# Kernel optimization log

Hardware: AMD Instinct MI355X
Metric: run time of the kernel (lower is better)

The kernel has to match this reference:

```python
import jax, jax.numpy as jnp
import numpy as np

EPS = 1e-8
WINDOW = 3      # config.router_window_size
TEMP = 1.0      # config.router_temp (> 0, so sqrt(D) fallback unused)
TOP_K = 2       # config.moe_top_k


def _routing_weights(x, prototypes):
    # L2-normalize router input per token (normalize_router_input=True)
    x = x / jnp.clip(jnp.linalg.norm(x, axis=-1, keepdims=True), EPS)
    # 'window' mode: causal moving average of size WINDOW along seq, with the
    # first token replicated WINDOW-1 times on the left (matches F.conv1d with
    # left pad of flat_input[:, :, [0]] and an averaging kernel).
    w = WINDOW
    padded = jnp.concatenate([jnp.repeat(x[:, :1], w - 1, axis=1), x], axis=1)  # [B, S+w-1, D]
    cs = jnp.concatenate(
        [jnp.zeros_like(padded[:, :1]), jnp.cumsum(padded, axis=1)], axis=1
    )  # [B, S+w, D]
    router_input = (cs[:, w:] - cs[:, :-w]) / w  # [B, S, D] moving mean
    # F.linear(router_input, prototypes): logits over experts
    logits = jnp.einsum('bsd,ed->bse', router_input, prototypes)  # [B, S, E]
    # softmax in float32 (F.softmax(..., dtype=torch.float))
    return jax.nn.softmax((logits / TEMP).astype(jnp.float32), axis=-1)


def setup_inputs() -> dict:
    key = jax.random.key(0)
    k1, k2 = jax.random.split(key)
    bs, sq, D, E = 8, 2048, 1024, 64
    x = jax.random.normal(k1, (bs, sq, D), dtype=jnp.float32)
    prototypes = jax.random.normal(k2, (E, D), dtype=jnp.float32) * 0.02
    attn_mask = jnp.ones((bs, sq), dtype=jnp.int32)
    return {"x": x, "prototypes": prototypes, "attn_mask": attn_mask}


def reference(x, prototypes, attn_mask):
    # attn_mask is all ones here; in 'window' mode it only feeds logging stats.
    routing_weights = _routing_weights(x, prototypes)          # [B, S, E]
    weights, modules = jax.lax.top_k(routing_weights, TOP_K)   # [B, S, K]
    weights = weights / weights.sum(axis=-1, keepdims=True)    # renormalize top-k
    return modules, weights
```

## Files before the change

### kernel.cpp

```cpp
#include <hip/hip_runtime.h>
#include <math.h>


#define BB 8
#define SS 2048
#define DD 1024
#define EE 64
#define EPSV 1e-8f

#define FMA4(A, s, P) \
  A.x += (s) * (P).x; A.y += (s) * (P).y; A.z += (s) * (P).z; A.w += (s) * (P).w;

#define SUMSQ4(v) ((v).x * (v).x + (v).y * (v).y + (v).z * (v).z + (v).w * (v).w)

__global__ __launch_bounds__(256) void repack_proto(
    const float* __restrict__ proto, float* __restrict__ ptt) {
  const int gid = blockIdx.x * 256 + threadIdx.x;
  const int d = gid >> 6;
  const int e = gid & 63;
  ptt[gid] = proto[(size_t)e * DD + d];
}

__global__ __launch_bounds__(512) void router_dots(
    const float* __restrict__ x, const float* __restrict__ ptt,
    float* __restrict__ dots) {
  __shared__ float SMEM[9216];

  const int tid  = threadIdx.x;
  const int lane = tid & 63;
  const int w    = __builtin_amdgcn_readfirstlane(tid >> 6);
  const int eg   = lane & 7;
  const int tg   = lane >> 3;
  const int b    = blockIdx.x >> 5;
  const int s0   = (blockIdx.x & 31) * 64;

  float* xtw = SMEM + w * 544;
  float* ptw = SMEM + 4352 + w * 512;
  float* nqp = SMEM + 8704;

  const int kbase = w * 128;
  const float* xsrow = x + ((size_t)b * SS + s0 + lane) * DD + kbase;
  const float* psrow = ptt + (size_t)kbase * EE + lane * 4;

  float4 accA0[4], accA1[4], accB0[4], accB1[4];
#pragma unroll
  for (int i = 0; i < 4; ++i) {
    accA0[i] = make_float4(0.f, 0.f, 0.f, 0.f);
    accA1[i] = make_float4(0.f, 0.f, 0.f, 0.f);
    accB0[i] = make_float4(0.f, 0.f, 0.f, 0.f);
    accB1[i] = make_float4(0.f, 0.f, 0.f, 0.f);
  }
  float q = 0.0f;

  {
    const float4 v0 = *(const float4*)(xsrow);
    const float4 v1 = *(const float4*)(xsrow + 4);
    const float4 r0 = *(const float4*)(psrow);
    const float4 r1 = *(const float4*)(psrow + 256);
    q += SUMSQ4(v0) + SUMSQ4(v1);
    float* d = xtw + lane;
    d[0]   = v0.x; d[68]  = v0.y; d[136] = v0.z; d[204] = v0.w;
    d[272] = v1.x; d[340] = v1.y; d[408] = v1.z; d[476] = v1.w;
    *(float4*)(ptw + lane * 4)       = r0;
    *(float4*)(ptw + 256 + lane * 4) = r1;
  }

  const float* xc = xtw + tg * 8;
  const float* pc = ptw + eg * 8;

  for (int c = 0; c < 16; ++c) {
    float4 v0, v1, r0, r1;
    if (c + 1 < 16) {
      v0 = *(const float4*)(xsrow + (c + 1) * 8);
      v1 = *(const float4*)(xsrow + (c + 1) * 8 + 4);
      r0 = *(const float4*)(psrow + (c + 1) * 512);
      r1 = *(const float4*)(psrow + (c + 1) * 512 + 256);
    }
#pragma unroll
    for (int kk = 0; kk < 8; ++kk) {
      const float4 xfA = *(const float4*)(xc + kk * 68);
      const float4 xfB = *(const float4*)(xc + kk * 68 + 4);
      const float4 p0  = *(const float4*)(pc + kk * 64);
      const float4 p1  = *(const float4*)(pc + kk * 64 + 4);
      FMA4(accA0[0], xfA.x, p0) FMA4(accA1[0], xfA.x, p1)
      FMA4(accA0[1], xfA.y, p0) FMA4(accA1[1], xfA.y, p1)
      FMA4(accA0[2], xfA.z, p0) FMA4(accA1[2], xfA.z, p1)
      FMA4(accA0[3], xfA.w, p0) FMA4(accA1[3], xfA.w, p1)
      FMA4(accB0[0], xfB.x, p0) FMA4(accB1[0], xfB.x, p1)
      FMA4(accB0[1], xfB.y, p0) FMA4(accB1[1], xfB.y, p1)
      FMA4(accB0[2], xfB.z, p0) FMA4(accB1[2], xfB.z, p1)
      FMA4(accB0[3], xfB.w, p0) FMA4(accB1[3], xfB.w, p1)
    }
    if (c + 1 < 16) {
      q += SUMSQ4(v0) + SUMSQ4(v1);
      float* d = xtw + lane;
      d[0]   = v0.x; d[68]  = v0.y; d[136] = v0.z; d[204] = v0.w;
      d[272] = v1.x; d[340] = v1.y; d[408] = v1.z; d[476] = v1.w;
      *(float4*)(ptw + lane * 4)       = r0;
      *(float4*)(ptw + 256 + lane * 4) = r1;
    }
  }

  nqp[w * 64 + lane] = q;

  float* B0 = SMEM;
  float* B1 = SMEM + 4352;

#define WRB(R)                                                        \
  { _Pragma("unroll") for (int i = 0; i < 4; ++i) {                   \
      float* pA_ = (R) + (tg * 8 + i) * 68 + eg * 8;                  \
      float* pB_ = (R) + (tg * 8 + 4 + i) * 68 + eg * 8;              \
      *(float4*)(pA_)     = accA0[i];                                 \
      *(float4*)(pA_ + 4) = accA1[i];                                 \
      *(float4*)(pB_)     = accB0[i];                                 \
      *(float4*)(pB_ + 4) = accB1[i]; } }
#define ADDB(R)                                                       \
  { _Pragma("unroll") for (int i = 0; i < 4; ++i) {                   \
      const float* pA_ = (R) + (tg * 8 + i) * 68 + eg * 8;            \
      const float* pB_ = (R) + (tg * 8 + 4 + i) * 68 + eg * 8;        \
      const float4 tA0 = *(const float4*)(pA_);                       \
      const float4 tA1 = *(const float4*)(pA_ + 4);                   \
      const float4 tB0 = *(const float4*)(pB_);                       \
      const float4 tB1 = *(const float4*)(pB_ + 4);                   \
      accA0[i].x += tA0.x; accA0[i].y += tA0.y;                       \
      accA0[i].z += tA0.z; accA0[i].w += tA0.w;                       \
      accA1[i].x += tA1.x; accA1[i].y += tA1.y;                       \
      accA1[i].z += tA1.z; accA1[i].w += tA1.w;                       \
      accB0[i].x += tB0.x; accB0[i].y += tB0.y;                       \
      accB0[i].z += tB0.z; accB0[i].w += tB0.w;                       \
      accB1[i].x += tB1.x; accB1[i].y += tB1.y;                       \
      accB1[i].z += tB1.z; accB1[i].w += tB1.w; } }

  __syncthreads();
  if (w == 1) WRB(B0)
  if (w == 5) WRB(B1)
  __syncthreads();
  if (w == 0) ADDB(B0)
  if (w == 4) ADDB(B1)
  __syncthreads();
  if (w == 3) WRB(B0)
  if (w == 7) WRB(B1)
  __syncthreads();
  if (w == 2) ADDB(B0)
  if (w == 6) ADDB(B1)
  __syncthreads();
  if (w == 2) WRB(B0)
  if (w == 6) WRB(B1)
  __syncthreads();
  if (w == 0) ADDB(B0)
  if (w == 4) ADDB(B1)
  __syncthreads();
  if (w == 4) WRB(B0)
  __syncthreads();
  if (w == 0) {
    ADDB(B0)
#pragma unroll
    for (int i = 0; i < 4; ++i) {
      const int rA = tg * 8 + i;
      const int rB = rA + 4;
      float qsA = 0.0f, qsB = 0.0f;
#pragma unroll
      for (int ww = 0; ww < 8; ++ww) {
        qsA += nqp[ww * 64 + rA];
        qsB += nqp[ww * 64 + rB];
      }
      const float invA = 1.0f / fmaxf(sqrtf(qsA), EPSV);
      const float invB = 1.0f / fmaxf(sqrtf(qsB), EPSV);
      float4 oA0 = accA0[i], oA1 = accA1[i], oB0 = accB0[i], oB1 = accB1[i];
      oA0.x *= invA; oA0.y *= invA; oA0.z *= invA; oA0.w *= invA;
      oA1.x *= invA; oA1.y *= invA; oA1.z *= invA; oA1.w *= invA;
      oB0.x *= invB; oB0.y *= invB; oB0.z *= invB; oB0.w *= invB;
      oB1.x *= invB; oB1.y *= invB; oB1.z *= invB; oB1.w *= invB;
      float* dpA = dots + ((size_t)b * SS + s0 + rA) * EE + eg * 8;
      float* dpB = dots + ((size_t)b * SS + s0 + rB) * EE + eg * 8;
      *(float4*)(dpA)     = oA0;
      *(float4*)(dpA + 4) = oA1;
      *(float4*)(dpB)     = oB0;
      *(float4*)(dpB + 4) = oB1;
    }
  }
}

#define T2UP(s, ei)                                            \
  if ((s) > v1) { v2 = v1; i2 = i1; v1 = (s); i1 = (ei); }     \
  else if ((s) > v2) { v2 = (s); i2 = (ei); }

__global__ __launch_bounds__(256) void router_top2(
    const float* __restrict__ dots, float* __restrict__ out) {
  const int gtid = blockIdx.x * 256 + threadIdx.x;
  const int tok  = gtid >> 3;
  const int h    = gtid & 7;
  const int b    = tok >> 11;
  const int sl   = tok & (SS - 1);
  const int r0   = (sl >= 2) ? sl - 2 : 0;
  const int r1   = (sl >= 1) ? sl - 1 : 0;

  const float* d0 = dots + ((size_t)b * SS + r0) * EE + h * 8;
  const float* d1 = dots + ((size_t)b * SS + r1) * EE + h * 8;
  const float* d2 = dots + ((size_t)b * SS + sl) * EE + h * 8;

  float v1 = -INFINITY, v2 = -INFINITY;
  int i1 = 0, i2 = 0;
#pragma unroll
  for (int qd = 0; qd < 2; ++qd) {
    const float4 a = *(const float4*)(d0 + qd * 4);
    const float4 c = *(const float4*)(d1 + qd * 4);
    const float4 e = *(const float4*)(d2 + qd * 4);
    const int e0 = h * 8 + qd * 4;
    float s;
    s = a.x + c.x + e.x; T2UP(s, e0 + 0)
    s = a.y + c.y + e.y; T2UP(s, e0 + 1)
    s = a.z + c.z + e.z; T2UP(s, e0 + 2)
    s = a.w + c.w + e.w; T2UP(s, e0 + 3)
  }

#pragma unroll
  for (int m = 1; m <= 4; m <<= 1) {
    const float ov1 = __shfl_xor(v1, m);
    const int   oi1 = __shfl_xor(i1, m);
    const float ov2 = __shfl_xor(v2, m);
    const int   oi2 = __shfl_xor(i2, m);
    const bool o_beats = (ov1 > v1) || (ov1 == v1 && oi1 < i1);
    if (o_beats) {
      const bool v1_beats_o2 = (v1 > ov2) || (v1 == ov2 && i1 < oi2);
      v2 = v1_beats_o2 ? v1 : ov2;
      i2 = v1_beats_o2 ? i1 : oi2;
      v1 = ov1;
      i1 = oi1;
    } else {
      const bool o1_beats_v2 = (ov1 > v2) || (ov1 == v2 && oi1 < i2);
      if (o1_beats_v2) { v2 = ov1; i2 = oi1; }
    }
  }

  if (h == 0) {
    const float ex = expf((v2 - v1) * (1.0f / 3.0f));
    const float w1 = 1.0f / (1.0f + ex);
    const size_t o = (size_t)tok * 2;
    *(float2*)(out + o) = make_float2((float)i1, (float)i2);
    *(float2*)(out + (size_t)BB * SS * 2 + o) = make_float2(w1, ex * w1);
  }
}

extern "C" void kernel_launch(void* const* d_in, const int* in_sizes, int n_in,
                              void* d_out, int out_size, void* d_ws, size_t ws_size,
                              hipStream_t stream) {
  const float* x     = (const float*)d_in[0];
  const float* proto = (const float*)d_in[1];
  float* out  = (float*)d_out;
  float* ptt  = (float*)d_ws;
  float* dots = (float*)((char*)d_ws + (512 << 10));

  repack_proto<<<dim3(256), dim3(256), 0, stream>>>(proto, ptt);
  router_dots<<<dim3(256), dim3(512), 0, stream>>>(x, ptt, dots);
  router_top2<<<dim3(512), dim3(256), 0, stream>>>(dots, out);
}
```

Baseline: 126.8 us.

## Split router dot K-dimension across sixteen waves per block instead of eight

The router_dots kernel now launches 1024 threads per block, and each of 16 waves handles a 64-wide slice of D instead of a 128-wide slice, halving the per-wave inner loop. Shared memory grows to hold the extra per-wave tiles, and the cross-wave reduction tree is extended to 16 partial sums. The aim is more memory-level parallelism per CU, since the grid has only 256 blocks. The cost is more reduction stages with extra barriers, plus tighter register limits under the larger launch bound.

```diff
diff --git a/kernel.cpp b/kernel.cpp
--- a/kernel.cpp
+++ b/kernel.cpp
@@ -21,10 +21,10 @@
   ptt[gid] = proto[(size_t)e * DD + d];
 }
 
-__global__ __launch_bounds__(512) void router_dots(
+__global__ __launch_bounds__(1024) void router_dots(
     const float* __restrict__ x, const float* __restrict__ ptt,
     float* __restrict__ dots) {
-  __shared__ float SMEM[9216];
+  __shared__ float SMEM[17920];
 
   const int tid  = threadIdx.x;
   const int lane = tid & 63;
@@ -35,10 +35,10 @@
   const int s0   = (blockIdx.x & 31) * 64;
 
   float* xtw = SMEM + w * 544;
-  float* ptw = SMEM + 4352 + w * 512;
-  float* nqp = SMEM + 8704;
-
-  const int kbase = w * 128;
+  float* ptw = SMEM + 8704 + w * 512;
+  float* nqp = SMEM + 16896;
+
+  const int kbase = w * 64;
   const float* xsrow = x + ((size_t)b * SS + s0 + lane) * DD + kbase;
   const float* psrow = ptt + (size_t)kbase * EE + lane * 4;
 
@@ -68,9 +68,9 @@
   const float* xc = xtw + tg * 8;
   const float* pc = ptw + eg * 8;
 
-  for (int c = 0; c < 16; ++c) {
+  for (int c = 0; c < 8; ++c) {
     float4 v0, v1, r0, r1;
-    if (c + 1 < 16) {
+    if (c + 1 < 8) {
       v0 = *(const float4*)(xsrow + (c + 1) * 8);
       v1 = *(const float4*)(xsrow + (c + 1) * 8 + 4);
       r0 = *(const float4*)(psrow + (c + 1) * 512);
@@ -91,7 +91,7 @@
       FMA4(accB0[2], xfB.z, p0) FMA4(accB1[2], xfB.z, p1)
       FMA4(accB0[3], xfB.w, p0) FMA4(accB1[3], xfB.w, p1)
     }
-    if (c + 1 < 16) {
+    if (c + 1 < 8) {
       q += SUMSQ4(v0) + SUMSQ4(v1);
       float* d = xtw + lane;
       d[0]   = v0.x; d[68]  = v0.y; d[136] = v0.z; d[204] = v0.w;
@@ -132,25 +132,35 @@
       accB1[i].z += tB1.z; accB1[i].w += tB1.w; } }
 
   __syncthreads();
-  if (w == 1) WRB(B0)
-  if (w == 5) WRB(B1)
-  __syncthreads();
-  if (w == 0) ADDB(B0)
-  if (w == 4) ADDB(B1)
-  __syncthreads();
-  if (w == 3) WRB(B0)
-  if (w == 7) WRB(B1)
-  __syncthreads();
-  if (w == 2) ADDB(B0)
-  if (w == 6) ADDB(B1)
-  __syncthreads();
-  if (w == 2) WRB(B0)
-  if (w == 6) WRB(B1)
-  __syncthreads();
-  if (w == 0) ADDB(B0)
-  if (w == 4) ADDB(B1)
-  __syncthreads();
-  if (w == 4) WRB(B0)
+  if (w == 1) WRB(B0)   if (w == 5) WRB(B1)
+  __syncthreads();
+  if (w == 0) ADDB(B0)  if (w == 4) ADDB(B1)
+  __syncthreads();
+  if (w == 3) WRB(B0)   if (w == 7) WRB(B1)
+  __syncthreads();
+  if (w == 2) ADDB(B0)  if (w == 6) ADDB(B1)
+  __syncthreads();
+  if (w == 9) WRB(B0)   if (w == 13) WRB(B1)
+  __syncthreads();
+  if (w == 8) ADDB(B0)  if (w == 12) ADDB(B1)
+  __syncthreads();
+  if (w == 11) WRB(B0)  if (w == 15) WRB(B1)
+  __syncthreads();
+  if (w == 10) ADDB(B0) if (w == 14) ADDB(B1)
+  __syncthreads();
+  if (w == 2) WRB(B0)   if (w == 6) WRB(B1)
+  __syncthreads();
+  if (w == 0) ADDB(B0)  if (w == 4) ADDB(B1)
+  __syncthreads();
+  if (w == 10) WRB(B0)  if (w == 14) WRB(B1)
+  __syncthreads();
+  if (w == 8) ADDB(B0)  if (w == 12) ADDB(B1)
+  __syncthreads();
+  if (w == 4) WRB(B0)   if (w == 12) WRB(B1)
+  __syncthreads();
+  if (w == 0) ADDB(B0)  if (w == 8) ADDB(B1)
+  __syncthreads();
+  if (w == 8) WRB(B0)
   __syncthreads();
   if (w == 0) {
     ADDB(B0)
@@ -160,7 +170,7 @@
       const int rB = rA + 4;
       float qsA = 0.0f, qsB = 0.0f;
 #pragma unroll
-      for (int ww = 0; ww < 8; ++ww) {
+      for (int ww = 0; ww < 16; ++ww) {
         qsA += nqp[ww * 64 + rA];
         qsB += nqp[ww * 64 + rB];
       }
@@ -252,6 +262,6 @@
   float* dots = (float*)((char*)d_ws + (512 << 10));
 
   repack_proto<<<dim3(256), dim3(256), 0, stream>>>(proto, ptt);
-  router_dots<<<dim3(256), dim3(512), 0, stream>>>(x, ptt, dots);
+  router_dots<<<dim3(256), dim3(1024), 0, stream>>>(x, ptt, dots);
   router_top2<<<dim3(512), dim3(256), 0, stream>>>(dots, out);
 }
```

Result: slower. 485.7 us (+282.9%).

## Split the router dot-product K dimension across two blocks per token tile

Applied to the files above, without the earlier changes.

The router_dots grid doubles from 256 to 512 blocks, each block handling half of the 1024-wide feature dimension. Each half writes unnormalized partial dot products and partial squared norms to workspace. The top-2 kernel then sums the halves and applies the per-token normalization. This is meant to fill more compute units on a GPU with many CUs, at the cost of twice the intermediate writes and reads plus extra work in the final kernel.

```diff
diff --git a/kernel.cpp b/kernel.cpp
--- a/kernel.cpp
+++ b/kernel.cpp
@@ -23,7 +23,7 @@
 
 __global__ __launch_bounds__(512) void router_dots(
     const float* __restrict__ x, const float* __restrict__ ptt,
-    float* __restrict__ dots) {
+    float* __restrict__ pdots, float* __restrict__ qpart) {
   __shared__ float SMEM[9216];
 
   const int tid  = threadIdx.x;
@@ -31,14 +31,16 @@
   const int w    = __builtin_amdgcn_readfirstlane(tid >> 6);
   const int eg   = lane & 7;
   const int tg   = lane >> 3;
-  const int b    = blockIdx.x >> 5;
-  const int s0   = (blockIdx.x & 31) * 64;
+  const int hb   = blockIdx.x & 1;
+  const int tb   = blockIdx.x >> 1;
+  const int b    = tb >> 5;
+  const int s0   = (tb & 31) * 64;
 
   float* xtw = SMEM + w * 544;
   float* ptw = SMEM + 4352 + w * 512;
   float* nqp = SMEM + 8704;
 
-  const int kbase = w * 128;
+  const int kbase = hb * 512 + w * 64;
   const float* xsrow = x + ((size_t)b * SS + s0 + lane) * DD + kbase;
   const float* psrow = ptt + (size_t)kbase * EE + lane * 4;
 
@@ -68,9 +70,9 @@
   const float* xc = xtw + tg * 8;
   const float* pc = ptw + eg * 8;
 
-  for (int c = 0; c < 16; ++c) {
+  for (int c = 0; c < 8; ++c) {
     float4 v0, v1, r0, r1;
-    if (c + 1 < 16) {
+    if (c + 1 < 8) {
       v0 = *(const float4*)(xsrow + (c + 1) * 8);
       v1 = *(const float4*)(xsrow + (c + 1) * 8 + 4);
       r0 = *(const float4*)(psrow + (c + 1) * 512);
@@ -91,7 +93,7 @@
       FMA4(accB0[2], xfB.z, p0) FMA4(accB1[2], xfB.z, p1)
       FMA4(accB0[3], xfB.w, p0) FMA4(accB1[3], xfB.w, p1)
     }
-    if (c + 1 < 16) {
+    if (c + 1 < 8) {
       q += SUMSQ4(v0) + SUMSQ4(v1);
       float* d = xtw + lane;
       d[0]   = v0.x; d[68]  = v0.y; d[136] = v0.z; d[204] = v0.w;
@@ -154,29 +156,32 @@
   __syncthreads();
   if (w == 0) {
     ADDB(B0)
+    const size_t half = (size_t)BB * SS * EE;
 #pragma unroll
     for (int i = 0; i < 4; ++i) {
       const int rA = tg * 8 + i;
       const int rB = rA + 4;
-      float qsA = 0.0f, qsB = 0.0f;
-#pragma unroll
-      for (int ww = 0; ww < 8; ++ww) {
-        qsA += nqp[ww * 64 + rA];
-        qsB += nqp[ww * 64 + rB];
+      float* dpA = pdots + hb * half + ((size_t)b * SS + s0 + rA) * EE + eg * 8;
+      float* dpB = pdots + hb * half + ((size_t)b * SS + s0 + rB) * EE + eg * 8;
+      *(float4*)(dpA)     = accA0[i];
+      *(float4*)(dpA + 4) = accA1[i];
+      *(float4*)(dpB)     = accB0[i];
+      *(float4*)(dpB + 4) = accB1[i];
+    }
+    if (eg == 0) {
+#pragma unroll
+      for (int i = 0; i < 4; ++i) {
+        const int rA = tg * 8 + i;
+        const int rB = rA + 4;
+        float qsA = 0.0f, qsB = 0.0f;
+#pragma unroll
+        for (int ww = 0; ww < 8; ++ww) {
+          qsA += nqp[ww * 64 + rA];
+          qsB += nqp[ww * 64 + rB];
+        }
+        qpart[hb * (size_t)(BB * SS) + (size_t)b * SS + s0 + rA] = qsA;
+        qpart[hb * (size_t)(BB * SS) + (size_t)b * SS + s0 + rB] = qsB;
       }
-      const float invA = 1.0f / fmaxf(sqrtf(qsA), EPSV);
-      const float invB = 1.0f / fmaxf(sqrtf(qsB), EPSV);
-      float4 oA0 = accA0[i], oA1 = accA1[i], oB0 = accB0[i], oB1 = accB1[i];
-      oA0.x *= invA; oA0.y *= invA; oA0.z *= invA; oA0.w *= invA;
-      oA1.x *= invA; oA1.y *= invA; oA1.z *= invA; oA1.w *= invA;
-      oB0.x *= invB; oB0.y *= invB; oB0.z *= invB; oB0.w *= invB;
-      oB1.x *= invB; oB1.y *= invB; oB1.z *= invB; oB1.w *= invB;
-      float* dpA = dots + ((size_t)b * SS + s0 + rA) * EE + eg * 8;
-      float* dpB = dots + ((size_t)b * SS + s0 + rB) * EE + eg * 8;
-      *(float4*)(dpA)     = oA0;
-      *(float4*)(dpA + 4) = oA1;
-      *(float4*)(dpB)     = oB0;
-      *(float4*)(dpB + 4) = oB1;
     }
   }
 }
@@ -186,7 +191,8 @@
   else if ((s) > v2) { v2 = (s); i2 = (ei); }
 
 __global__ __launch_bounds__(256) void router_top2(
-    const float* __restrict__ dots, float* __restrict__ out) {
+    const float* __restrict__ pdots, const float* __restrict__ qpart,
+    float* __restrict__ out) {
   const int gtid = blockIdx.x * 256 + threadIdx.x;
   const int tok  = gtid >> 3;
   const int h    = gtid & 7;
@@ -195,23 +201,43 @@
   const int r0   = (sl >= 2) ? sl - 2 : 0;
   const int r1   = (sl >= 1) ? sl - 1 : 0;
 
-  const float* d0 = dots + ((size_t)b * SS + r0) * EE + h * 8;
-  const float* d1 = dots + ((size_t)b * SS + r1) * EE + h * 8;
-  const float* d2 = dots + ((size_t)b * SS + sl) * EE + h * 8;
+  const size_t half = (size_t)BB * SS * EE;
+  const size_t rb   = (size_t)b * SS;
+
+  const float inv0 =
+      1.0f / fmaxf(sqrtf(qpart[rb + r0] + qpart[(size_t)BB * SS + rb + r0]), EPSV);
+  const float inv1 =
+      1.0f / fmaxf(sqrtf(qpart[rb + r1] + qpart[(size_t)BB * SS + rb + r1]), EPSV);
+  const float inv2 =
+      1.0f / fmaxf(sqrtf(qpart[rb + sl] + qpart[(size_t)BB * SS + rb + sl]), EPSV);
+
+  const float* a0 = pdots + (rb + r0) * EE + h * 8;
+  const float* a1 = pdots + half + (rb + r0) * EE + h * 8;
+  const float* c0 = pdots + (rb + r1) * EE + h * 8;
+  const float* c1 = pdots + half + (rb + r1) * EE + h * 8;
+  const float* e0p = pdots + (rb + sl) * EE + h * 8;
+  const float* e1p = pdots + half + (rb + sl) * EE + h * 8;
 
   float v1 = -INFINITY, v2 = -INFINITY;
   int i1 = 0, i2 = 0;
 #pragma unroll
   for (int qd = 0; qd < 2; ++qd) {
-    const float4 a = *(const float4*)(d0 + qd * 4);
-    const float4 c = *(const float4*)(d1 + qd * 4);
-    const float4 e = *(const float4*)(d2 + qd * 4);
-    const int e0 = h * 8 + qd * 4;
+    const float4 aL = *(const float4*)(a0 + qd * 4);
+    const float4 aH = *(const float4*)(a1 + qd * 4);
+    const float4 cL = *(const float4*)(c0 + qd * 4);
+    const float4 cH = *(const float4*)(c1 + qd * 4);
+    const float4 eL = *(const float4*)(e0p + qd * 4);
+    const float4 eH = *(const float4*)(e1p + qd * 4);
+    const int ei = h * 8 + qd * 4;
     float s;
-    s = a.x + c.x + e.x; T2UP(s, e0 + 0)
-    s = a.y + c.y + e.y; T2UP(s, e0 + 1)
-    s = a.z + c.z + e.z; T2UP(s, e0 + 2)
-    s = a.w + c.w + e.w; T2UP(s, e0 + 3)
+    s = (aL.x + aH.x) * inv0 + (cL.x + cH.x) * inv1 + (eL.x + eH.x) * inv2;
+    T2UP(s, ei + 0)
+    s = (aL.y + aH.y) * inv0 + (cL.y + cH.y) * inv1 + (eL.y + eH.y) * inv2;
+    T2UP(s, ei + 1)
+    s = (aL.z + aH.z) * inv0 + (cL.z + cH.z) * inv1 + (eL.z + eH.z) * inv2;
+    T2UP(s, ei + 2)
+    s = (aL.w + aH.w) * inv0 + (cL.w + cH.w) * inv1 + (eL.w + eH.w) * inv2;
+    T2UP(s, ei + 3)
   }
 
 #pragma unroll
@@ -247,11 +273,12 @@
                               hipStream_t stream) {
   const float* x     = (const float*)d_in[0];
   const float* proto = (const float*)d_in[1];
-  float* out  = (float*)d_out;
-  float* ptt  = (float*)d_ws;
-  float* dots = (float*)((char*)d_ws + (512 << 10));
+  float* out   = (float*)d_out;
+  float* ptt   = (float*)d_ws;
+  float* pdots = (float*)((char*)d_ws + (512 << 10));
+  float* qpart = (float*)((char*)d_ws + (512 << 10) + (8 << 20));
 
   repack_proto<<<dim3(256), dim3(256), 0, stream>>>(proto, ptt);
-  router_dots<<<dim3(256), dim3(512), 0, stream>>>(x, ptt, dots);
-  router_top2<<<dim3(512), dim3(256), 0, stream>>>(dots, out);
-}
+  router_dots<<<dim3(512), dim3(512), 0, stream>>>(x, ptt, pdots, qpart);
+  router_top2<<<dim3(512), dim3(256), 0, stream>>>(pdots, qpart, out);
+}
```

After: 146.2 us. 15.3% more time.

## Fuse top-2 selection into router dot kernel with halo token recompute

Applied to the files above, without the earlier changes.

Merges the dot-product and top-2 kernels into one. Each 64-token block also recomputes the normalized dots for the two preceding tokens (halo) using scalar loads and per-lane FMA, so the 3-token window sum can be done from shared memory. This removes the dots round-trip through global memory and one kernel launch. In exchange it adds redundant halo work, extra uncoalesced global loads and shared-memory use, and one more barrier.

```diff
diff --git a/kernel.cpp b/kernel.cpp
--- a/kernel.cpp
+++ b/kernel.cpp
@@ -21,10 +21,10 @@
   ptt[gid] = proto[(size_t)e * DD + d];
 }
 
-__global__ __launch_bounds__(512) void router_dots(
+__global__ __launch_bounds__(512, 1) void fused_router(
     const float* __restrict__ x, const float* __restrict__ ptt,
-    float* __restrict__ dots) {
-  __shared__ float SMEM[9216];
+    float* __restrict__ out) {
+  __shared__ float SMEM[10256];
 
   const int tid  = threadIdx.x;
   const int lane = tid & 63;
@@ -37,10 +37,17 @@
   float* xtw = SMEM + w * 544;
   float* ptw = SMEM + 4352 + w * 512;
   float* nqp = SMEM + 8704;
+  float* hpp = SMEM + 9216;
+  float* hqq = SMEM + 10240;
 
   const int kbase = w * 128;
   const float* xsrow = x + ((size_t)b * SS + s0 + lane) * DD + kbase;
   const float* psrow = ptt + (size_t)kbase * EE + lane * 4;
+
+  const int g0 = (s0 >= 2) ? s0 - 2 : 0;
+  const int g1 = (s0 >= 1) ? s0 - 1 : 0;
+  const float* xh0 = x + ((size_t)b * SS + g0) * DD + kbase;
+  const float* xh1 = x + ((size_t)b * SS + g1) * DD + kbase;
 
   float4 accA0[4], accA1[4], accB0[4], accB1[4];
 #pragma unroll
@@ -51,6 +58,8 @@
     accB1[i] = make_float4(0.f, 0.f, 0.f, 0.f);
   }
   float q = 0.0f;
+  float ha0 = 0.0f, ha1 = 0.0f;
+  float hs0 = 0.0f, hs1 = 0.0f;
 
   {
     const float4 v0 = *(const float4*)(xsrow);
@@ -75,6 +84,12 @@
       v1 = *(const float4*)(xsrow + (c + 1) * 8 + 4);
       r0 = *(const float4*)(psrow + (c + 1) * 512);
       r1 = *(const float4*)(psrow + (c + 1) * 512 + 256);
+    }
+    float h0v[8], h1v[8];
+#pragma unroll
+    for (int kk = 0; kk < 8; ++kk) {
+      h0v[kk] = xh0[c * 8 + kk];
+      h1v[kk] = xh1[c * 8 + kk];
     }
 #pragma unroll
     for (int kk = 0; kk < 8; ++kk) {
@@ -91,6 +106,14 @@
       FMA4(accB0[2], xfB.z, p0) FMA4(accB1[2], xfB.z, p1)
       FMA4(accB0[3], xfB.w, p0) FMA4(accB1[3], xfB.w, p1)
     }
+#pragma unroll
+    for (int kk = 0; kk < 8; ++kk) {
+      const float pv = ptw[kk * 64 + lane];
+      ha0 += h0v[kk] * pv;
+      ha1 += h1v[kk] * pv;
+      hs0 += h0v[kk] * h0v[kk];
+      hs1 += h1v[kk] * h1v[kk];
+    }
     if (c + 1 < 16) {
       q += SUMSQ4(v0) + SUMSQ4(v1);
       float* d = xtw + lane;
@@ -102,6 +125,9 @@
   }
 
   nqp[w * 64 + lane] = q;
+  hpp[w * 128 + lane]      = ha0;
+  hpp[w * 128 + 64 + lane] = ha1;
+  if (lane == 0) { hqq[w * 2] = hs0; hqq[w * 2 + 1] = hs1; }
 
   float* B0 = SMEM;
   float* B1 = SMEM + 4352;
@@ -152,8 +178,10 @@
   __syncthreads();
   if (w == 4) WRB(B0)
   __syncthreads();
+  if (w == 0) ADDB(B0)
+  __syncthreads();
+
   if (w == 0) {
-    ADDB(B0)
 #pragma unroll
     for (int i = 0; i < 4; ++i) {
       const int rA = tg * 8 + i;
@@ -171,74 +199,86 @@
       oA1.x *= invA; oA1.y *= invA; oA1.z *= invA; oA1.w *= invA;
       oB0.x *= invB; oB0.y *= invB; oB0.z *= invB; oB0.w *= invB;
       oB1.x *= invB; oB1.y *= invB; oB1.z *= invB; oB1.w *= invB;
-      float* dpA = dots + ((size_t)b * SS + s0 + rA) * EE + eg * 8;
-      float* dpB = dots + ((size_t)b * SS + s0 + rB) * EE + eg * 8;
-      *(float4*)(dpA)     = oA0;
-      *(float4*)(dpA + 4) = oA1;
-      *(float4*)(dpB)     = oB0;
-      *(float4*)(dpB + 4) = oB1;
-    }
-  }
-}
+      float* TA = SMEM + (2 + rA) * 68 + eg * 8;
+      float* TB = SMEM + (2 + rB) * 68 + eg * 8;
+      *(float4*)(TA)     = oA0;
+      *(float4*)(TA + 4) = oA1;
+      *(float4*)(TB)     = oB0;
+      *(float4*)(TB + 4) = oB1;
+    }
+  }
+  if (w == 1) {
+    float d0 = 0.f, d1 = 0.f, q0 = 0.f, q1 = 0.f;
+#pragma unroll
+    for (int ww = 0; ww < 8; ++ww) {
+      d0 += hpp[ww * 128 + lane];
+      d1 += hpp[ww * 128 + 64 + lane];
+      q0 += hqq[ww * 2];
+      q1 += hqq[ww * 2 + 1];
+    }
+    SMEM[lane]      = d0 * (1.0f / fmaxf(sqrtf(q0), EPSV));
+    SMEM[68 + lane] = d1 * (1.0f / fmaxf(sqrtf(q1), EPSV));
+  }
+  __syncthreads();
 
 #define T2UP(s, ei)                                            \
   if ((s) > v1) { v2 = v1; i2 = i1; v1 = (s); i1 = (ei); }     \
   else if ((s) > v2) { v2 = (s); i2 = (ei); }
 
-__global__ __launch_bounds__(256) void router_top2(
-    const float* __restrict__ dots, float* __restrict__ out) {
-  const int gtid = blockIdx.x * 256 + threadIdx.x;
-  const int tok  = gtid >> 3;
-  const int h    = gtid & 7;
-  const int b    = tok >> 11;
-  const int sl   = tok & (SS - 1);
-  const int r0   = (sl >= 2) ? sl - 2 : 0;
-  const int r1   = (sl >= 1) ? sl - 1 : 0;
-
-  const float* d0 = dots + ((size_t)b * SS + r0) * EE + h * 8;
-  const float* d1 = dots + ((size_t)b * SS + r1) * EE + h * 8;
-  const float* d2 = dots + ((size_t)b * SS + sl) * EE + h * 8;
-
-  float v1 = -INFINITY, v2 = -INFINITY;
-  int i1 = 0, i2 = 0;
-#pragma unroll
-  for (int qd = 0; qd < 2; ++qd) {
-    const float4 a = *(const float4*)(d0 + qd * 4);
-    const float4 c = *(const float4*)(d1 + qd * 4);
-    const float4 e = *(const float4*)(d2 + qd * 4);
-    const int e0 = h * 8 + qd * 4;
-    float s;
-    s = a.x + c.x + e.x; T2UP(s, e0 + 0)
-    s = a.y + c.y + e.y; T2UP(s, e0 + 1)
-    s = a.z + c.z + e.z; T2UP(s, e0 + 2)
-    s = a.w + c.w + e.w; T2UP(s, e0 + 3)
-  }
-
-#pragma unroll
-  for (int m = 1; m <= 4; m <<= 1) {
-    const float ov1 = __shfl_xor(v1, m);
-    const int   oi1 = __shfl_xor(i1, m);
-    const float ov2 = __shfl_xor(v2, m);
-    const int   oi2 = __shfl_xor(i2, m);
-    const bool o_beats = (ov1 > v1) || (ov1 == v1 && oi1 < i1);
-    if (o_beats) {
-      const bool v1_beats_o2 = (v1 > ov2) || (v1 == ov2 && i1 < oi2);
-      v2 = v1_beats_o2 ? v1 : ov2;
-      i2 = v1_beats_o2 ? i1 : oi2;
-      v1 = ov1;
-      i1 = oi1;
-    } else {
-      const bool o1_beats_v2 = (ov1 > v2) || (ov1 == v2 && oi1 < i2);
-      if (o1_beats_v2) { v2 = ov1; i2 = oi1; }
-    }
-  }
-
-  if (h == 0) {
-    const float ex = expf((v2 - v1) * (1.0f / 3.0f));
-    const float w1 = 1.0f / (1.0f + ex);
-    const size_t o = (size_t)tok * 2;
-    *(float2*)(out + o) = make_float2((float)i1, (float)i2);
-    *(float2*)(out + (size_t)BB * SS * 2 + o) = make_float2(w1, ex * w1);
+  {
+    const int t   = tid >> 3;
+    const int oct = tid & 7;
+    int ra = t, rb = t + 1;
+    if (s0 == 0) {
+      ra = (t < 2) ? 2 : t;
+      rb = (t == 0) ? 2 : t + 1;
+    }
+    const float* Ta = SMEM + ra * 68 + oct * 8;
+    const float* Tb = SMEM + rb * 68 + oct * 8;
+    const float* Tc = SMEM + (t + 2) * 68 + oct * 8;
+
+    float v1 = -INFINITY, v2 = -INFINITY;
+    int i1 = 0, i2 = 0;
+#pragma unroll
+    for (int qd = 0; qd < 2; ++qd) {
+      const float4 a = *(const float4*)(Ta + qd * 4);
+      const float4 c = *(const float4*)(Tb + qd * 4);
+      const float4 e = *(const float4*)(Tc + qd * 4);
+      const int e0 = oct * 8 + qd * 4;
+      float s;
+      s = a.x + c.x + e.x; T2UP(s, e0 + 0)
+      s = a.y + c.y + e.y; T2UP(s, e0 + 1)
+      s = a.z + c.z + e.z; T2UP(s, e0 + 2)
+      s = a.w + c.w + e.w; T2UP(s, e0 + 3)
+    }
+
+#pragma unroll
+    for (int m = 1; m <= 4; m <<= 1) {
+      const float ov1 = __shfl_xor(v1, m);
+      const int   oi1 = __shfl_xor(i1, m);
+      const float ov2 = __shfl_xor(v2, m);
+      const int   oi2 = __shfl_xor(i2, m);
+      const bool o_beats = (ov1 > v1) || (ov1 == v1 && oi1 < i1);
+      if (o_beats) {
+        const bool v1_beats_o2 = (v1 > ov2) || (v1 == ov2 && i1 < oi2);
+        v2 = v1_beats_o2 ? v1 : ov2;
+        i2 = v1_beats_o2 ? i1 : oi2;
+        v1 = ov1;
+        i1 = oi1;
+      } else {
+        const bool o1_beats_v2 = (ov1 > v2) || (ov1 == v2 && oi1 < i2);
+        if (o1_beats_v2) { v2 = ov1; i2 = oi1; }
+      }
+    }
+
+    if (oct == 0) {
+      const float ex = expf((v2 - v1) * (1.0f / 3.0f));
+      const float w1 = 1.0f / (1.0f + ex);
+      const size_t gt = (size_t)b * SS + s0 + t;
+      const size_t o = gt * 2;
+      *(float2*)(out + o) = make_float2((float)i1, (float)i2);
+      *(float2*)(out + (size_t)BB * SS * 2 + o) = make_float2(w1, ex * w1);
+    }
   }
 }
 
@@ -247,11 +287,9 @@
                               hipStream_t stream) {
   const float* x     = (const float*)d_in[0];
   const float* proto = (const float*)d_in[1];
-  float* out  = (float*)d_out;
-  float* ptt  = (float*)d_ws;
-  float* dots = (float*)((char*)d_ws + (512 << 10));
+  float* out = (float*)d_out;
+  float* ptt = (float*)d_ws;
 
   repack_proto<<<dim3(256), dim3(256), 0, stream>>>(proto, ptt);
-  router_dots<<<dim3(256), dim3(512), 0, stream>>>(x, ptt, dots);
-  router_top2<<<dim3(512), dim3(256), 0, stream>>>(dots, out);
+  fused_router<<<dim3(256), dim3(512), 0, stream>>>(x, ptt, out);
 }
```

After: 123.6 us. -2.5%, faster.
